# Kernel optimization log

Hardware: AMD Instinct MI355X
Metric: run time of the kernel (lower is better)

Reference implementation:

```python
import jax, jax.numpy as jnp
import numpy as np
from jax import lax

V, E, H, K, T, B = 32000, 512, 512, 32, 256, 64
PAD_W = 0          # word_dict['PAD']
START, END, PAD_L = 30, 31, 0   # label_dict
NEG = -100000.0


def setup_inputs() -> dict:
    key = jax.random.key(0)
    ks = jax.random.split(key, 12)
    s = 1.0 / np.sqrt(H)
    tokens = jax.random.randint(ks[0], (T, B), 1, V, dtype=jnp.int32)   # >PAD_W -> mask all ones
    tags = jax.random.randint(ks[1], (T, B), 1, K - 2, dtype=jnp.int32)
    lengths = jnp.full((B,), T, dtype=jnp.int32)
    embed = jax.random.normal(ks[2], (V, E), jnp.float32) * 0.1
    wih0 = jax.random.uniform(ks[3], (2, 4 * H, E), jnp.float32, -s, s)
    whh0 = jax.random.uniform(ks[4], (2, 4 * H, H), jnp.float32, -s, s)
    b0 = jax.random.uniform(ks[5], (2, 4 * H), jnp.float32, -s, s)
    wih1 = jax.random.uniform(ks[6], (2, 4 * H, 2 * H), jnp.float32, -s, s)
    whh1 = jax.random.uniform(ks[7], (2, 4 * H, H), jnp.float32, -s, s)
    b1 = jax.random.uniform(ks[8], (2, 4 * H), jnp.float32, -s, s)
    lin_w = jax.random.uniform(ks[9], (K, 2 * H), jnp.float32, -s, s)
    lin_b = jax.random.uniform(ks[10], (K,), jnp.float32, -s, s)
    trans = jax.random.normal(ks[11], (K, K), jnp.float32)
    # replicate the torch transition init (same order of assignments)
    trans = trans.at[START, :].set(NEG)
    trans = trans.at[:, END].set(NEG)
    trans = trans.at[:, PAD_L].set(NEG)
    trans = trans.at[PAD_L, :].set(NEG)
    trans = trans.at[PAD_L, END].set(0.0)
    trans = trans.at[PAD_L, PAD_L].set(0.0)
    return dict(tokens=tokens, tags=tags, lengths=lengths, embed=embed,
                wih0=wih0, whh0=whh0, b0=b0, wih1=wih1, whh1=whh1, b1=b1,
                lin_w=lin_w, lin_b=lin_b, trans=trans)


def _lstm_dir(x, w_ih, w_hh, b, reverse):
    # x: [T,B,in] -> hs: [T,B,H]; gates precomputed as one big GEMM
    xp = jnp.einsum('tbi,gi->tbg', x, w_ih) + b  # [T,B,4H]
    h0 = jnp.zeros((x.shape[1], H), x.dtype)

    def step(carry, g_in):
        h, c = carry
        g = g_in + h @ w_hh.T
        i, f, gg, o = jnp.split(g, 4, axis=-1)  # torch gate order i,f,g,o
        c = jax.nn.sigmoid(f) * c + jax.nn.sigmoid(i) * jnp.tanh(gg)
        h = jax.nn.sigmoid(o) * jnp.tanh(c)
        return (h, c), h

    _, hs = lax.scan(step, (h0, h0), xp, reverse=reverse)
    return hs


def _bilstm_layer(x, wih, whh, b):
    return jnp.concatenate([_lstm_dir(x, wih[0], whh[0], b[0], False),
                            _lstm_dir(x, wih[1], whh[1], b[1], True)], axis=-1)


def reference(tokens, tags, lengths, embed, wih0, whh0, b0, wih1, whh1, b1,
              lin_w, lin_b, trans):
    mask = (tokens > PAD_W).astype(jnp.float32)  # [T,B]
    x = embed[tokens]                            # [T,B,E]
    x = _bilstm_layer(x, wih0, whh0, b0)
    x = _bilstm_layer(x, wih1, whh1, b1)
    feats = x @ lin_w.T + lin_b                  # [T,B,K]

    nB = tokens.shape[1]
    # ---- CRF forward algorithm: log Z(x) ----
    init = jnp.full((nB, K), NEG, feats.dtype).at[:, START].set(0.0)

    def step(score, inp):
        emit, m = inp  # [B,K], [B]
        # new[b,k] = logsumexp_j(score[b,j] + trans[k,j]) + emit[b,k]
        new = jax.nn.logsumexp(score[:, None, :] + trans[None, :, :], axis=2) + emit
        return jnp.where(m[:, None] > 0, new, score), None

    z, _ = lax.scan(step, init, (feats, mask))
    log_z = jax.nn.logsumexp(z + trans[END][None, :], axis=1)  # [B]

    # ---- gold path score (vectorized, masked deltas sum) ----
    start_row = jnp.full((1, nB), START, dtype=tags.dtype)
    te = jnp.concatenate([start_row, tags], axis=0)            # [T+1,B]
    trans_s = trans[te[1:], te[:-1]]                           # [T,B]
    emit_s = jnp.take_along_axis(feats, te[1:][..., None].astype(jnp.int32), axis=2)[..., 0]
    gold = jnp.sum(mask * (trans_s + emit_s), axis=0) + trans[END, te[-1]]

    return jnp.sum((log_z - gold) / lengths.astype(jnp.float32))
```

## Files before the change

kernel.cpp:

```cpp
#include <hip/hip_runtime.h>
#include <math.h>

#define T_STEPS 256
#define BATCH   64
#define HID     512
#define KTAGS   32
#define NEGV    -100000.0f
#define START_TAG 30
#define END_TAG   31

#define NBLK      256
#define SPIN_LIM  (1 << 26)
#define LAYER_DONE  300u
#define POISON_DONE 301u
#define POISON    0xFFFFFFFFFFFFFFFFULL

typedef __attribute__((ext_vector_type(8))) short short8;
typedef __attribute__((ext_vector_type(4))) float f32x4;

union V16 { uint4 u; short8 s; };
union HQ  { unsigned long long q[2]; short8 s; };

static __device__ __forceinline__ unsigned short f2b(float f) {
    unsigned u = __float_as_uint(f);
    return (unsigned short)((u + 0x7fffu + ((u >> 16) & 1u)) >> 16);
}
static __device__ __forceinline__ float b2f(unsigned short us) {
    return __uint_as_float(((unsigned)us) << 16);
}

__global__ __launch_bounds__(256) void init_zero(unsigned int* __restrict__ flags,
                                                 unsigned long long* __restrict__ hbuf,
                                                 float* __restrict__ out)
{
    int i = blockIdx.x * 256 + threadIdx.x;
    if (i < 131072)
        __hip_atomic_store(hbuf + i, POISON, __ATOMIC_RELAXED, __HIP_MEMORY_SCOPE_AGENT);
    if (i < 16384)
        __hip_atomic_store(flags + i, 0u, __ATOMIC_RELAXED, __HIP_MEMORY_SCOPE_AGENT);
    if (i == 0)
        __hip_atomic_store(out, 0.0f, __ATOMIC_RELAXED, __HIP_MEMORY_SCOPE_AGENT);
}

__global__ __launch_bounds__(256) void convert_embed(const float* __restrict__ src,
                                                     unsigned short* __restrict__ dst)
{
    long long i = ((long long)blockIdx.x * 256 + threadIdx.x) * 4;
    if (i >= (long long)32000 * 512) return;
    float4 v = *(const float4*)(src + i);
    ushort4 o;
    o.x = f2b(v.x); o.y = f2b(v.y); o.z = f2b(v.z); o.w = f2b(v.w);
    *(ushort4*)(dst + i) = o;
}

__global__ __launch_bounds__(256) void pack_w(const float* __restrict__ wih,
                                              const float* __restrict__ whh,
                                              int xK,
                                              unsigned short* __restrict__ wpack)
{
    const int xKt = xK >> 5, KT = xKt + 16;
    long long t = (long long)blockIdx.x * 256 + threadIdx.x;
    if (t >= (long long)2 * 64 * KT * 2 * 64) return;
    int lane = (int)(t & 63);
    long long rest = t >> 6;
    int nf = (int)(rest & 1); rest >>= 1;
    int kt = (int)(rest % KT); rest /= KT;
    int nt = (int)(rest % 64);
    int d  = (int)(rest / 64);
    int c = lane & 15, q = lane >> 4;
    int bc = nf * 16 + c;
    int r = (bc >> 3) * 512 + nt * 8 + (bc & 7);
    const float* src;
    if (kt < xKt) src = wih + ((long long)d * 2048 * xK + (long long)r * xK + kt * 32 + q * 8);
    else          src = whh + ((long long)d * 2048 * 512 + (long long)r * 512 + (kt - xKt) * 32 + q * 8);
    float4 v0 = *(const float4*)src;
    float4 v1 = *(const float4*)(src + 4);
    unsigned short o[8] = { f2b(v0.x), f2b(v0.y), f2b(v0.z), f2b(v0.w),
                            f2b(v1.x), f2b(v1.y), f2b(v1.z), f2b(v1.w) };
    *(uint4*)(wpack + t * 8) = *(const uint4*)o;
}

template<int XK>
static __device__ __forceinline__ void layer_steps(
    const int d, const int bg, const int nt, const int tid,
    const int* __restrict__ tokens,
    const unsigned short* __restrict__ embB,
    const unsigned short* __restrict__ hs_in,
    const unsigned short* __restrict__ wp,
    const float* __restrict__ bia,
    unsigned short* __restrict__ hso,
    unsigned long long* __restrict__ hbuf64,
    uint4* __restrict__ wlds,
    float (&Gred)[4][32][33],
    int* __restrict__ tok_s)
{
    constexpr bool L0  = (XK == 512);
    constexpr int  xKt = XK >> 5;
    constexpr int  KT  = xKt + 16;
    constexpr int  nX  = xKt >> 2;

    const int w = tid >> 6, lane = tid & 63;
    const int lm = lane & 15, q = lane >> 4;
    const int brow = tid >> 3, hc = tid & 7;

    const uint4* wp4 = (const uint4*)wp;
    for (int j = tid; j < KT * 128; j += 256)
        wlds[j] = wp4[j];

    float breg[4];
    #pragma unroll
    for (int g = 0; g < 4; ++g) breg[g] = bia[g * 512 + nt * 8 + hc];
    float creg = 0.0f;

    __syncthreads();

    for (int s = 0; s < T_STEPS; ++s) {
        const int tt = d ? (T_STEPS - 1 - s) : s;

        if (L0 && tid < 32) tok_s[tid] = tokens[tt * BATCH + bg * 32 + tid];
        __syncthreads();

        const unsigned short* xr[2];
        #pragma unroll
        for (int mt = 0; mt < 2; ++mt) {
            int m = mt * 16 + lm;
            if (L0) xr[mt] = embB + (long long)tok_s[m] * 512;
            else    xr[mt] = hs_in + ((long long)tt * 64 + bg * 32 + m) * 1024;
        }

        uint4 av[nX][2];
        #pragma unroll
        for (int i = 0; i < nX; ++i) {
            const int kt = w * nX + i;
            #pragma unroll
            for (int mt = 0; mt < 2; ++mt)
                av[i][mt] = *(const uint4*)(xr[mt] + kt * 32 + q * 8);
        }

        HQ hq[4][2];
        const unsigned long long* hbq =
            hbuf64 + (long long)(((((s - 1) & 7) * 2 + d) * 2 + bg)) * 4096;
        if (s > 0) {
            #pragma unroll
            for (int i = 0; i < 4; ++i) {
                const int kth = w * 4 + i;
                #pragma unroll
                for (int mt = 0; mt < 2; ++mt) {
                    const int base = (kth * 4 + q) * 64 + (mt * 16 + lm) * 2;
                    hq[i][mt].q[0] = __hip_atomic_load(hbq + base,     __ATOMIC_RELAXED, __HIP_MEMORY_SCOPE_AGENT);
                    hq[i][mt].q[1] = __hip_atomic_load(hbq + base + 1, __ATOMIC_RELAXED, __HIP_MEMORY_SCOPE_AGENT);
                }
            }
        }

        f32x4 acc[2][2];
        #pragma unroll
        for (int mt = 0; mt < 2; ++mt)
            #pragma unroll
            for (int nf = 0; nf < 2; ++nf) acc[mt][nf] = (f32x4)0.0f;

        #pragma unroll
        for (int i = 0; i < nX; ++i) {
            const int kt = w * nX + i;
            V16 a0, a1, b0, b1;
            a0.u = av[i][0]; a1.u = av[i][1];
            b0.u = wlds[(kt * 2 + 0) * 64 + lane];
            b1.u = wlds[(kt * 2 + 1) * 64 + lane];
            acc[0][0] = __builtin_amdgcn_mfma_f32_16x16x32_bf16(a0.s, b0.s, acc[0][0], 0, 0, 0);
            acc[0][1] = __builtin_amdgcn_mfma_f32_16x16x32_bf16(a0.s, b1.s, acc[0][1], 0, 0, 0);
            acc[1][0] = __builtin_amdgcn_mfma_f32_16x16x32_bf16(a1.s, b0.s, acc[1][0], 0, 0, 0);
            acc[1][1] = __builtin_amdgcn_mfma_f32_16x16x32_bf16(a1.s, b1.s, acc[1][1], 0, 0, 0);
        }

        if (s > 0) {
            #pragma unroll
            for (int i = 0; i < 4; ++i) {
                const int kth = w * 4 + i;
                int n = 0;
                for (;;) {
                    int bad = 0;
                    #pragma unroll
                    for (int mt = 0; mt < 2; ++mt) {
                        const int base = (kth * 4 + q) * 64 + (mt * 16 + lm) * 2;
                        if (hq[i][mt].q[0] == POISON) {
                            hq[i][mt].q[0] = __hip_atomic_load(hbq + base,     __ATOMIC_RELAXED, __HIP_MEMORY_SCOPE_AGENT);
                            bad = 1;
                        }
                        if (hq[i][mt].q[1] == POISON) {
                            hq[i][mt].q[1] = __hip_atomic_load(hbq + base + 1, __ATOMIC_RELAXED, __HIP_MEMORY_SCOPE_AGENT);
                            bad = 1;
                        }
                    }
                    if (!bad) break;
                    __builtin_amdgcn_s_sleep(1);
                    if (++n > SPIN_LIM) break;
                }
                V16 b0, b1;
                b0.u = wlds[((xKt + kth) * 2 + 0) * 64 + lane];
                b1.u = wlds[((xKt + kth) * 2 + 1) * 64 + lane];
                acc[0][0] = __builtin_amdgcn_mfma_f32_16x16x32_bf16(hq[i][0].s, b0.s, acc[0][0], 0, 0, 0);
                acc[0][1] = __builtin_amdgcn_mfma_f32_16x16x32_bf16(hq[i][0].s, b1.s, acc[0][1], 0, 0, 0);
                acc[1][0] = __builtin_amdgcn_mfma_f32_16x16x32_bf16(hq[i][1].s, b0.s, acc[1][0], 0, 0, 0);
                acc[1][1] = __builtin_amdgcn_mfma_f32_16x16x32_bf16(hq[i][1].s, b1.s, acc[1][1], 0, 0, 0);
            }
        }

        #pragma unroll
        for (int mt = 0; mt < 2; ++mt)
            #pragma unroll
            for (int nf = 0; nf < 2; ++nf)
                #pragma unroll
                for (int r = 0; r < 4; ++r)
                    Gred[w][nf * 16 + lm][mt * 16 + q * 4 + r] = acc[mt][nf][r];
        __syncthreads();

        float vg[4];
        #pragma unroll
        for (int g = 0; g < 4; ++g) {
            float v = breg[g];
            #pragma unroll
            for (int ww = 0; ww < 4; ++ww) v += Gred[ww][g * 8 + hc][brow];
            vg[g] = v;
        }
        const float si = 1.0f / (1.0f + __expf(-vg[0]));
        const float sf = 1.0f / (1.0f + __expf(-vg[1]));
        const float so = 1.0f / (1.0f + __expf(-vg[3]));
        const float cn = sf * creg + si * tanhf(vg[2]);
        const float hn = so * tanhf(cn);
        creg = cn;

        unsigned pv = (unsigned)f2b(hn);
        unsigned p2 = pv | (__shfl_xor(pv, 1) << 16);
        unsigned long long hv = (unsigned long long)p2
                              | ((unsigned long long)__shfl_xor(p2, 2) << 32);
        if ((tid & 3) == 0) {
            const int row = brow, cq = hc >> 2;
            unsigned long long* dst =
                hbuf64 + ((long long)((((s & 7) * 2 + d) * 2 + bg) * 64 + nt)) * 64 + row * 2 + cq;
            __hip_atomic_store(dst, hv, __ATOMIC_RELAXED, __HIP_MEMORY_SCOPE_AGENT);
            *(unsigned long long*)(hso + ((long long)tt * 64 + bg * 32 + row) * 1024
                                       + d * 512 + nt * 8 + cq * 4) = hv;
            unsigned long long* pdst =
                hbuf64 + ((long long)(((((s + 2) & 7) * 2 + d) * 2 + bg) * 64 + nt)) * 64 + row * 2 + cq;
            __hip_atomic_store(pdst, POISON, __ATOMIC_RELAXED, __HIP_MEMORY_SCOPE_AGENT);
        }
    }
}

__global__ __launch_bounds__(256, 1) void lstm_mfma(
    const int* __restrict__ tokens,
    const unsigned short* __restrict__ embB,
    const unsigned short* __restrict__ wp0,
    const unsigned short* __restrict__ wp1,
    const float* __restrict__ bb0, const float* __restrict__ bb1,
    unsigned short* __restrict__ hs0,
    unsigned short* __restrict__ hs1,
    unsigned long long* __restrict__ hbuf64,
    unsigned int* __restrict__ flags)
{
    __shared__ uint4 wlds[6144];
    __shared__ float Gred[4][32][33];
    __shared__ int   tok_s[32];

    const int bid = blockIdx.x;
    const int d   = bid >> 7;
    const int bg  = (bid >> 6) & 1;
    const int nt  = bid & 63;
    const int tid = threadIdx.x;

    layer_steps<512>(d, bg, nt, tid, tokens, embB, (const unsigned short*)nullptr,
                     wp0 + (long long)(d * 64 + nt) * 32 * 1024,
                     bb0 + (long long)d * 2048,
                     hs0, hbuf64, wlds, Gred, tok_s);

    {
        __threadfence();
        __syncthreads();
        if (tid == 0)
            __hip_atomic_store(flags + bid * 32, LAYER_DONE,
                               __ATOMIC_RELAXED, __HIP_MEMORY_SCOPE_AGENT);
        if (tid < 64) {
            int n = 0;
            for (;;) {
                unsigned a = __hip_atomic_load(flags + tid * 32,         __ATOMIC_RELAXED, __HIP_MEMORY_SCOPE_AGENT);
                unsigned b = __hip_atomic_load(flags + (tid + 64) * 32,  __ATOMIC_RELAXED, __HIP_MEMORY_SCOPE_AGENT);
                unsigned c = __hip_atomic_load(flags + (tid + 128) * 32, __ATOMIC_RELAXED, __HIP_MEMORY_SCOPE_AGENT);
                unsigned e = __hip_atomic_load(flags + (tid + 192) * 32, __ATOMIC_RELAXED, __HIP_MEMORY_SCOPE_AGENT);
                if (__all(a >= LAYER_DONE && b >= LAYER_DONE &&
                          c >= LAYER_DONE && e >= LAYER_DONE)) break;
                __builtin_amdgcn_s_sleep(1);
                if (++n > SPIN_LIM) break;
            }
        }
        __syncthreads();
        if (tid < 64) {
            #pragma unroll
            for (int p = 0; p < 8; ++p) {
                unsigned long long* pd =
                    hbuf64 + ((long long)(((p * 2 + d) * 2 + bg) * 64 + nt)) * 64 + tid;
                __hip_atomic_store(pd, POISON, __ATOMIC_RELAXED, __HIP_MEMORY_SCOPE_AGENT);
            }
        }
        asm volatile("s_waitcnt vmcnt(0)" ::: "memory");
        __syncthreads();
        if (tid == 0)
            __hip_atomic_store(flags + bid * 32, POISON_DONE,
                               __ATOMIC_RELAXED, __HIP_MEMORY_SCOPE_AGENT);
        if (tid < 64) {
            int n = 0;
            for (;;) {
                unsigned a = __hip_atomic_load(flags + tid * 32,         __ATOMIC_RELAXED, __HIP_MEMORY_SCOPE_AGENT);
                unsigned b = __hip_atomic_load(flags + (tid + 64) * 32,  __ATOMIC_RELAXED, __HIP_MEMORY_SCOPE_AGENT);
                unsigned c = __hip_atomic_load(flags + (tid + 128) * 32, __ATOMIC_RELAXED, __HIP_MEMORY_SCOPE_AGENT);
                unsigned e = __hip_atomic_load(flags + (tid + 192) * 32, __ATOMIC_RELAXED, __HIP_MEMORY_SCOPE_AGENT);
                if (__all(a >= POISON_DONE && b >= POISON_DONE &&
                          c >= POISON_DONE && e >= POISON_DONE)) break;
                __builtin_amdgcn_s_sleep(1);
                if (++n > SPIN_LIM) break;
            }
        }
        __syncthreads();
        __threadfence();
    }

    layer_steps<1024>(d, bg, nt, tid, tokens, embB, hs0,
                      wp1 + (long long)(d * 64 + nt) * 48 * 1024,
                      bb1 + (long long)d * 2048,
                      hs1, hbuf64, wlds, Gred, tok_s);
}

__global__ __launch_bounds__(256) void gemm_feats(
    const unsigned short* __restrict__ A,
    const float* __restrict__ W,
    const float* __restrict__ bias,
    float* __restrict__ C,
    int M, int N, int K)
{
    __shared__ __align__(16) float As[64][34];
    __shared__ __align__(16) float Ws[32][68];

    const int m0 = blockIdx.y * 64;
    const int tid = threadIdx.x;
    const int tr = tid >> 4;
    const int tc = tid & 15;

    float acc[4][4];
    #pragma unroll
    for (int i = 0; i < 4; ++i)
        #pragma unroll
        for (int j = 0; j < 4; ++j) acc[i][j] = 0.0f;

    for (int k0 = 0; k0 < K; k0 += 32) {
        {
            int row = tid >> 2, g8 = tid & 3;
            uint4 v = *(const uint4*)(A + ((long long)(m0 + row)) * 1024 + k0 + g8 * 8);
            const unsigned short* pv = (const unsigned short*)&v;
            #pragma unroll
            for (int e = 0; e < 8; ++e) As[row][g8 * 8 + e] = b2f(pv[e]);
        }
        {
            int row = tid >> 3, q2 = tid & 7;
            float4 v = *(const float4*)(W + (long long)row * K + k0 + 4 * q2);
            Ws[4*q2+0][row] = v.x; Ws[4*q2+1][row] = v.y;
            Ws[4*q2+2][row] = v.z; Ws[4*q2+3][row] = v.w;
        }
        __syncthreads();
        #pragma unroll 8
        for (int kk = 0; kk < 32; ++kk) {
            float a0 = As[4*tr+0][kk], a1 = As[4*tr+1][kk];
            float a2 = As[4*tr+2][kk], a3 = As[4*tr+3][kk];
            float4 wv = *(const float4*)&Ws[kk][4*tc];
            acc[0][0] += a0*wv.x; acc[0][1] += a0*wv.y; acc[0][2] += a0*wv.z; acc[0][3] += a0*wv.w;
            acc[1][0] += a1*wv.x; acc[1][1] += a1*wv.y; acc[1][2] += a1*wv.z; acc[1][3] += a1*wv.w;
            acc[2][0] += a2*wv.x; acc[2][1] += a2*wv.y; acc[2][2] += a2*wv.z; acc[2][3] += a2*wv.w;
            acc[3][0] += a3*wv.x; acc[3][1] += a3*wv.y; acc[3][2] += a3*wv.z; acc[3][3] += a3*wv.w;
        }
        __syncthreads();
    }
    #pragma unroll
    for (int i = 0; i < 4; ++i) {
        int m = m0 + 4*tr + i;
        #pragma unroll
        for (int j = 0; j < 4; ++j) {
            int n = 4*tc + j;
            if (n < N) C[(long long)m * N + n] = acc[i][j] + bias[n];
        }
    }
}

__global__ __launch_bounds__(1024) void crf_kernel(
    const float* __restrict__ feats,
    const float* __restrict__ trans,
    const int*   __restrict__ tokens,
    const int*   __restrict__ tags,
    const int*   __restrict__ lengths,
    float* __restrict__ out)
{
    const int b = blockIdx.x;
    const int tid = threadIdx.x;
    __shared__ float tr_s[KTAGS*KTAGS];
    __shared__ float score_s[KTAGS];
    __shared__ float emit_s[KTAGS];
    __shared__ float red_s[16];
    __shared__ float logz_s;

    tr_s[tid] = trans[tid];
    if (tid < KTAGS) score_s[tid] = (tid == START_TAG) ? 0.0f : NEGV;
    __syncthreads();

    const int i = tid >> 5, j = tid & 31;
    for (int t = 0; t < T_STEPS; ++t) {
        if (tid < KTAGS) emit_s[tid] = feats[((long long)t*BATCH + b)*KTAGS + tid];
        __syncthreads();
        float e = score_s[j] + tr_s[i*KTAGS + j];
        float m = e;
        m = fmaxf(m, __shfl_xor(m, 1));  m = fmaxf(m, __shfl_xor(m, 2));
        m = fmaxf(m, __shfl_xor(m, 4));  m = fmaxf(m, __shfl_xor(m, 8));
        m = fmaxf(m, __shfl_xor(m, 16));
        float p = __expf(e - m);
        p += __shfl_xor(p, 1); p += __shfl_xor(p, 2); p += __shfl_xor(p, 4);
        p += __shfl_xor(p, 8); p += __shfl_xor(p, 16);
        float nv = m + __logf(p) + emit_s[i];
        int msk = tokens[(long long)t*BATCH + b] > 0;
        __syncthreads();
        if (j == 0) score_s[i] = msk ? nv : score_s[i];
        __syncthreads();
    }

    if (tid < KTAGS) {
        float v = score_s[tid] + tr_s[END_TAG*KTAGS + tid];
        float m = v;
        m = fmaxf(m, __shfl_xor(m, 1));  m = fmaxf(m, __shfl_xor(m, 2));
        m = fmaxf(m, __shfl_xor(m, 4));  m = fmaxf(m, __shfl_xor(m, 8));
        m = fmaxf(m, __shfl_xor(m, 16));
        float p = __expf(v - m);
        p += __shfl_xor(p, 1); p += __shfl_xor(p, 2); p += __shfl_xor(p, 4);
        p += __shfl_xor(p, 8); p += __shfl_xor(p, 16);
        if (tid == 0) logz_s = m + __logf(p);
    }
    __syncthreads();

    float val = 0.0f;
    if (tid < T_STEPS) {
        int t = tid;
        int cur  = tags[(long long)t*BATCH + b];
        int prev = (t == 0) ? START_TAG : tags[(long long)(t-1)*BATCH + b];
        int msk  = tokens[(long long)t*BATCH + b] > 0;
        if (msk) val = tr_s[cur*KTAGS + prev]
                     + feats[((long long)t*BATCH + b)*KTAGS + cur];
    }
    val += __shfl_xor(val, 1);  val += __shfl_xor(val, 2);
    val += __shfl_xor(val, 4);  val += __shfl_xor(val, 8);
    val += __shfl_xor(val, 16); val += __shfl_xor(val, 32);
    int wave = tid >> 6, lane = tid & 63;
    if (lane == 0) red_s[wave] = val;
    __syncthreads();
    if (tid == 0) {
        float g = 0.0f;
        #pragma unroll
        for (int w = 0; w < 16; ++w) g += red_s[w];
        g += tr_s[END_TAG*KTAGS + tags[(long long)(T_STEPS-1)*BATCH + b]];
        atomicAdd(out, (logz_s - g) / (float)lengths[b]);
    }
}

extern "C" void kernel_launch(void* const* d_in, const int* in_sizes, int n_in,
                              void* d_out, int out_size, void* d_ws, size_t ws_size,
                              hipStream_t stream) {
    const int*   tokens  = (const int*)  d_in[0];
    const int*   tags    = (const int*)  d_in[1];
    const int*   lengths = (const int*)  d_in[2];
    const float* embed   = (const float*)d_in[3];
    const float* wih0    = (const float*)d_in[4];
    const float* whh0    = (const float*)d_in[5];
    const float* b0      = (const float*)d_in[6];
    const float* wih1    = (const float*)d_in[7];
    const float* whh1    = (const float*)d_in[8];
    const float* b1      = (const float*)d_in[9];
    const float* lin_w   = (const float*)d_in[10];
    const float* lin_b   = (const float*)d_in[11];
    const float* trans   = (const float*)d_in[12];

    char* ws = (char*)d_ws;
    unsigned short* hs0   = (unsigned short*)(ws);
    unsigned short* hs1   = (unsigned short*)(ws +  33554432ULL);
    unsigned short* embB  = (unsigned short*)(ws +  67108864ULL);
    unsigned short* wp0   = (unsigned short*)(ws +  99876864ULL);
    unsigned short* wp1   = (unsigned short*)(ws + 108265472ULL);
    float*          feats = (float*)        (ws + 120848384ULL);
    unsigned int*   flagsP = (unsigned int*)feats;
    unsigned long long* hbufP = (unsigned long long*)((char*)feats + 65536);

    float* out = (float*)d_out;

    init_zero<<<dim3(512), 256, 0, stream>>>(flagsP, hbufP, out);
    convert_embed<<<dim3(16000), 256, 0, stream>>>(embed, embB);
    pack_w<<<dim3(2048), 256, 0, stream>>>(wih0, whh0, 512,  wp0);
    pack_w<<<dim3(3072), 256, 0, stream>>>(wih1, whh1, 1024, wp1);

    lstm_mfma<<<dim3(NBLK), 256, 0, stream>>>(
        tokens, embB, wp0, wp1, b0, b1, hs0, hs1, hbufP, flagsP);

    gemm_feats<<<dim3(1, 256, 1), 256, 0, stream>>>(
        hs1, lin_w, lin_b, feats, T_STEPS*BATCH, KTAGS, 2*HID);

    crf_kernel<<<dim3(BATCH), 1024, 0, stream>>>(feats, trans, tokens, tags,
                                                 lengths, out);
}
```

Measured before the change: 2.483 ms.

## Remove per-step token barrier, double-buffer gate reduction, batch h-polling across waves

```diff
diff --git a/kernel.cpp b/kernel.cpp
--- a/kernel.cpp
+++ b/kernel.cpp
@@ -10,7 +10,7 @@
 #define END_TAG   31
 
 #define NBLK      256
-#define SPIN_LIM  (1 << 26)
+#define SPIN_LIM  (1 << 24)
 #define LAYER_DONE  300u
 #define POISON_DONE 301u
 #define POISON    0xFFFFFFFFFFFFFFFFULL
@@ -91,8 +91,7 @@
     unsigned short* __restrict__ hso,
     unsigned long long* __restrict__ hbuf64,
     uint4* __restrict__ wlds,
-    float (&Gred)[4][32][33],
-    int* __restrict__ tok_s)
+    float (&Gred)[2][4][32][36])
 {
     constexpr bool L0  = (XK == 512);
     constexpr int  xKt = XK >> 5;
@@ -116,16 +115,18 @@
 
     for (int s = 0; s < T_STEPS; ++s) {
         const int tt = d ? (T_STEPS - 1 - s) : s;
-
-        if (L0 && tid < 32) tok_s[tid] = tokens[tt * BATCH + bg * 32 + tid];
-        __syncthreads();
+        const int p  = s & 1;
 
         const unsigned short* xr[2];
         #pragma unroll
         for (int mt = 0; mt < 2; ++mt) {
             int m = mt * 16 + lm;
-            if (L0) xr[mt] = embB + (long long)tok_s[m] * 512;
-            else    xr[mt] = hs_in + ((long long)tt * 64 + bg * 32 + m) * 1024;
+            if (L0) {
+                int tok = tokens[tt * BATCH + bg * 32 + m];
+                xr[mt] = embB + (long long)tok * 512;
+            } else {
+                xr[mt] = hs_in + ((long long)tt * 64 + bg * 32 + m) * 1024;
+            }
         }
 
         uint4 av[nX][2];
@@ -173,28 +174,32 @@
         }
 
         if (s > 0) {
-            #pragma unroll
-            for (int i = 0; i < 4; ++i) {
-                const int kth = w * 4 + i;
-                int n = 0;
-                for (;;) {
-                    int bad = 0;
+            int pass = 0;
+            for (;;) {
+                int ok = 1;
+                #pragma unroll
+                for (int i = 0; i < 4; ++i)
+                    #pragma unroll
+                    for (int mt = 0; mt < 2; ++mt)
+                        ok &= (hq[i][mt].q[0] != POISON) && (hq[i][mt].q[1] != POISON);
+                if (__all(ok)) break;
+                if (++pass > SPIN_LIM) break;
+                if (pass >= 3) __builtin_amdgcn_s_sleep(1);
+                #pragma unroll
+                for (int i = 0; i < 4; ++i) {
+                    const int kth = w * 4 + i;
                     #pragma unroll
                     for (int mt = 0; mt < 2; ++mt) {
                         const int base = (kth * 4 + q) * 64 + (mt * 16 + lm) * 2;
-                        if (hq[i][mt].q[0] == POISON) {
-                            hq[i][mt].q[0] = __hip_atomic_load(hbq + base,     __ATOMIC_RELAXED, __HIP_MEMORY_SCOPE_AGENT);
-                            bad = 1;
-                        }
-                        if (hq[i][mt].q[1] == POISON) {
-                            hq[i][mt].q[1] = __hip_atomic_load(hbq + base + 1, __ATOMIC_RELAXED, __HIP_MEMORY_SCOPE_AGENT);
-                            bad = 1;
-                        }
+                        hq[i][mt].q[0] = __hip_atomic_load(hbq + base,     __ATOMIC_RELAXED, __HIP_MEMORY_SCOPE_AGENT);
+                        hq[i][mt].q[1] = __hip_atomic_load(hbq + base + 1, __ATOMIC_RELAXED, __HIP_MEMORY_SCOPE_AGENT);
                     }
-                    if (!bad) break;
-                    __builtin_amdgcn_s_sleep(1);
-                    if (++n > SPIN_LIM) break;
                 }
+            }
+
+            #pragma unroll
+            for (int i = 0; i < 4; ++i) {
+                const int kth = w * 4 + i;
                 V16 b0, b1;
                 b0.u = wlds[((xKt + kth) * 2 + 0) * 64 + lane];
                 b1.u = wlds[((xKt + kth) * 2 + 1) * 64 + lane];
@@ -210,17 +215,24 @@
             #pragma unroll
             for (int nf = 0; nf < 2; ++nf)
                 #pragma unroll
-                for (int r = 0; r < 4; ++r)
-                    Gred[w][nf * 16 + lm][mt * 16 + q * 4 + r] = acc[mt][nf][r];
+                for (int r = 0; r < 4; ++r) {
+                    const int row = mt * 16 + q * 4 + r;
+                    const int c   = nf * 16 + lm;
+                    const int cp  = (c & 7) * 4 + (c >> 3);
+                    Gred[p][w][row][cp] = acc[mt][nf][r];
+                }
         __syncthreads();
 
         float vg[4];
-        #pragma unroll
-        for (int g = 0; g < 4; ++g) {
-            float v = breg[g];
-            #pragma unroll
-            for (int ww = 0; ww < 4; ++ww) v += Gred[ww][g * 8 + hc][brow];
-            vg[g] = v;
+        {
+            const float4 g0 = *(const float4*)&Gred[p][0][brow][hc * 4];
+            const float4 g1 = *(const float4*)&Gred[p][1][brow][hc * 4];
+            const float4 g2 = *(const float4*)&Gred[p][2][brow][hc * 4];
+            const float4 g3 = *(const float4*)&Gred[p][3][brow][hc * 4];
+            vg[0] = breg[0] + g0.x + g1.x + g2.x + g3.x;
+            vg[1] = breg[1] + g0.y + g1.y + g2.y + g3.y;
+            vg[2] = breg[2] + g0.z + g1.z + g2.z + g3.z;
+            vg[3] = breg[3] + g0.w + g1.w + g2.w + g3.w;
         }
         const float si = 1.0f / (1.0f + __expf(-vg[0]));
         const float sf = 1.0f / (1.0f + __expf(-vg[1]));
@@ -259,8 +271,7 @@
     unsigned int* __restrict__ flags)
 {
     __shared__ uint4 wlds[6144];
-    __shared__ float Gred[4][32][33];
-    __shared__ int   tok_s[32];
+    __shared__ __align__(16) float Gred[2][4][32][36];
 
     const int bid = blockIdx.x;
     const int d   = bid >> 7;
@@ -271,7 +282,7 @@
     layer_steps<512>(d, bg, nt, tid, tokens, embB, (const unsigned short*)nullptr,
                      wp0 + (long long)(d * 64 + nt) * 32 * 1024,
                      bb0 + (long long)d * 2048,
-                     hs0, hbuf64, wlds, Gred, tok_s);
+                     hs0, hbuf64, wlds, Gred);
 
     {
         __threadfence();
@@ -295,9 +306,9 @@
         __syncthreads();
         if (tid < 64) {
             #pragma unroll
-            for (int p = 0; p < 8; ++p) {
+            for (int pp = 0; pp < 8; ++pp) {
                 unsigned long long* pd =
-                    hbuf64 + ((long long)(((p * 2 + d) * 2 + bg) * 64 + nt)) * 64 + tid;
+                    hbuf64 + ((long long)(((pp * 2 + d) * 2 + bg) * 64 + nt)) * 64 + tid;
                 __hip_atomic_store(pd, POISON, __ATOMIC_RELAXED, __HIP_MEMORY_SCOPE_AGENT);
             }
         }
@@ -326,7 +337,7 @@
     layer_steps<1024>(d, bg, nt, tid, tokens, embB, hs0,
                       wp1 + (long long)(d * 64 + nt) * 48 * 1024,
                       bb1 + (long long)d * 2048,
-                      hs1, hbuf64, wlds, Gred, tok_s);
+                      hs1, hbuf64, wlds, Gred);
 }
 
 __global__ __launch_bounds__(256) void gemm_feats(
```

Result: faster. 2.312 ms (-6.9%).
